# Kernel tuning notes

Hardware: AMD Instinct MI355X
Metric: run time of the kernel (lower is better)

Reference implementation:

```python
import jax, jax.numpy as jnp
import numpy as np

DEPTH = 8          # complete binary tree: 2^8-1 = 255 internal nodes, 256 leaves
N_FEAT = 32
N_CLASSES = 10
BATCH = 131072


def setup_inputs() -> dict:
    key = jax.random.key(0)
    k_x, k_t, k_f, k_c = jax.random.split(key, 4)
    n_internal = (1 << DEPTH) - 1
    n_leaves = 1 << DEPTH
    x = jax.random.normal(k_x, (BATCH, N_FEAT), dtype=jnp.float32)
    # learnable per-node thresholds (initialized from the sklearn tree's thresholds)
    thresholds = jax.random.normal(k_t, (n_internal,), dtype=jnp.float32) * 0.5
    # non-differentiable split feature index per internal node
    feats = jax.random.randint(k_f, (n_internal,), 0, N_FEAT, dtype=jnp.int32)
    # majority class per leaf (argmax of sklearn value array)
    leaf_class = jax.random.randint(k_c, (n_leaves,), 0, N_CLASSES, dtype=jnp.int32)
    return {"x": x, "thresholds": thresholds, "feats": feats, "leaf_class": leaf_class}


def reference(x, thresholds, feats, leaf_class):
    # Soft decision-tree traversal. Internal nodes stored in level (heap) order:
    # level d occupies indices [2^d - 1, 2^(d+1) - 1). Children of the j-th node
    # of a level are the (2j)-th and (2j+1)-th nodes of the next level, so an
    # interleaved stack+reshape reproduces the heap child ordering exactly.
    B = x.shape[0]
    probs = jnp.ones((B, 1), dtype=x.dtype)  # root path probability
    start = 0
    for d in range(DEPTH):
        n = 1 << d
        f = feats[start:start + n]               # [n] split feature per node
        t = thresholds[start:start + n]          # [n] learnable threshold
        act = jax.nn.sigmoid(x[:, f] - t[None, :])   # [B, n] right-branch gate
        # left child gets (1 - act), right child gets act (matches _split_approx)
        probs = jnp.stack([probs * (1.0 - act), probs * act], axis=-1).reshape(B, 2 * n)
        start += n
    # sum leaf path probabilities per majority class (stack + sum in original)
    onehot = jax.nn.one_hot(leaf_class, N_CLASSES, dtype=x.dtype)  # [n_leaves, C]
    p = probs @ onehot                                             # [B, C]
    return p
```

## Files before the change

### kernel.cpp

```cpp
#include <hip/hip_runtime.h>


#define NFEAT 32
#define NCLS  10
#define TPB   256
#define RPB   256
#define XPITCH 258
#define L2E   1.4426950408889634f

typedef _Float16 f16x8 __attribute__((ext_vector_type(8)));
typedef float    f32x4 __attribute__((ext_vector_type(4)));

__device__ __forceinline__ float fexp2(float z) {
#if __has_builtin(__builtin_amdgcn_exp2f)
  return __builtin_amdgcn_exp2f(z);
#else
  return exp2f(z);
#endif
}
__device__ __forceinline__ float frcp(float z) {
#if __has_builtin(__builtin_amdgcn_rcpf)
  return __builtin_amdgcn_rcpf(z);
#else
  return 1.0f / z;
#endif
}
__device__ __forceinline__ float rlf(float v, int lane) {
  return __int_as_float(__builtin_amdgcn_readlane(__float_as_int(v), lane));
}
__device__ __forceinline__ int rli(int v, int lane) {
  return __builtin_amdgcn_readlane(v, lane);
}

struct NodeRegs {
  float ta, tb, t7;
  int   fa, fb, f7;
};

__device__ __forceinline__ void sig2(float tpow, int ft, const float* xT, int rp,
                                     float p0, float p1,
                                     float& l0, float& r0, float& l1, float& r1) {
  const float2 w = *(const float2*)&xT[ft * XPITCH + 2 * rp];
  const float a0 = frcp(__builtin_fmaf(tpow, w.x, 1.0f));
  const float a1 = frcp(__builtin_fmaf(tpow, w.y, 1.0f));
  r0 = p0 * a0;  l0 = p0 - r0;
  r1 = p1 * a1;  l1 = p1 - r1;
}
__device__ __forceinline__ void evalA2(const NodeRegs& R, const float* xT, int n,
                                       int rp, float p0, float p1,
                                       float& l0, float& r0, float& l1, float& r1) {
  sig2(rlf(R.ta, n), rli(R.fa, n), xT, rp, p0, p1, l0, r0, l1, r1);
}
__device__ __forceinline__ void evalB2(const NodeRegs& R, const float* xT, int n,
                                       int rp, float p0, float p1,
                                       float& l0, float& r0, float& l1, float& r1) {
  sig2(rlf(R.tb, n - 63), rli(R.fb, n - 63), xT, rp, p0, p1, l0, r0, l1, r1);
}
__device__ __forceinline__ void leafpair7x2(const NodeRegs& R, const float* xT,
                                            int l7, int rp, float p0, float p1,
                                            unsigned& u0, unsigned& u1) {
  float l0, r0, l1, r1;
  sig2(rlf(R.t7, l7), rli(R.f7, l7), xT, rp, p0, p1, l0, r0, l1, r1);
  const _Float16 hl0 = (_Float16)l0, hr0 = (_Float16)r0;
  const _Float16 hl1 = (_Float16)l1, hr1 = (_Float16)r1;
  u0 = ((unsigned)__builtin_bit_cast(unsigned short, hr0) << 16) |
        (unsigned)__builtin_bit_cast(unsigned short, hl0);
  u1 = ((unsigned)__builtin_bit_cast(unsigned short, hr1) << 16) |
        (unsigned)__builtin_bit_cast(unsigned short, hl1);
}

__device__ __forceinline__ void d5block2(const NodeRegs& R, const float* xT,
                                         int rp, int n5, int l7b,
                                         float p0, float p1,
                                         char* rowp0, char* rowp1,
                                         int boff0, int boff1) {
  float pl0, pr0, pl1, pr1;
  evalA2(R, xT, n5, rp, p0, p1, pl0, pr0, pl1, pr1);
  float qll0, qlr0, qll1, qlr1;
  evalB2(R, xT, 2 * n5 + 1, rp, pl0, pl1, qll0, qlr0, qll1, qlr1);
  float qrl0, qrr0, qrl1, qrr1;
  evalB2(R, xT, 2 * n5 + 2, rp, pr0, pr1, qrl0, qrr0, qrl1, qrr1);
  uint4 u0, u1;
  leafpair7x2(R, xT, l7b + 0, rp, qll0, qll1, u0.x, u1.x);
  leafpair7x2(R, xT, l7b + 1, rp, qlr0, qlr1, u0.y, u1.y);
  leafpair7x2(R, xT, l7b + 2, rp, qrl0, qrl1, u0.z, u1.z);
  leafpair7x2(R, xT, l7b + 3, rp, qrr0, qrr1, u0.w, u1.w);
  *(uint4*)(rowp0 + boff0) = u0;
  *(uint4*)(rowp1 + boff1) = u1;
}

__global__ __launch_bounds__(TPB, 2)
void dt_kernel(const float* __restrict__ x,
               const float* __restrict__ thr,
               const int*   __restrict__ feats,
               const int*   __restrict__ leafc,
               float*       __restrict__ out) {
  __shared__ __align__(16) float s_xT[NFEAT * XPITCH];
  __shared__ __align__(16) char  s_P[RPB * 128];
  __shared__ int s_lc[256];

  const int t    = threadIdx.x;
  const int lane = t & 63;
  const int rp   = t & 127;
  const int h    = t >> 7;

  NodeRegs R;
  R.ta = fexp2(thr[lane] * L2E);
  R.tb = fexp2(thr[63 + lane] * L2E);
  R.t7 = fexp2(thr[127 + 64 * h + lane] * L2E);
  R.fa = feats[lane];
  R.fb = feats[63 + lane];
  R.f7 = feats[127 + 64 * h + lane];

  const float4* xg = (const float4*)x + (size_t)blockIdx.x * (RPB * NFEAT / 4);
#pragma unroll
  for (int k = 0; k < 8; ++k) {
    const int i4 = k * TPB + t;
    const float4 v = xg[i4];
    const int r  = i4 >> 3;
    const int c0 = (i4 & 7) * 4;
    s_xT[(c0 + 0) * XPITCH + r] = fexp2(-v.x * L2E);
    s_xT[(c0 + 1) * XPITCH + r] = fexp2(-v.y * L2E);
    s_xT[(c0 + 2) * XPITCH + r] = fexp2(-v.z * L2E);
    s_xT[(c0 + 3) * XPITCH + r] = fexp2(-v.w * L2E);
  }
  s_lc[t] = leafc[t];

  __syncthreads();

  float pl0, pr0, pl1, pr1;
  evalA2(R, s_xT, 0, rp, 1.0f, 1.0f, pl0, pr0, pl1, pr1);
  const float pd10 = h ? pr0 : pl0;
  const float pd11 = h ? pr1 : pl1;
  evalA2(R, s_xT, 1 + h, rp, pd10, pd11, pl0, pr0, pl1, pr1);
  const float pA0 = pl0, pB0 = pr0, pA1 = pl1, pB1 = pr1;
  float pm00, pm01, pm02, pm03, pm10, pm11, pm12, pm13;
  evalA2(R, s_xT, 3 + 2 * h, rp, pA0, pA1, pm00, pm01, pm10, pm11);
  evalA2(R, s_xT, 4 + 2 * h, rp, pB0, pB1, pm02, pm03, pm12, pm13);

  const int row0 = 2 * rp, row1 = row0 + 1;
  const int swz0 = ((row0 ^ (row0 >> 3)) & 7) << 4;
  const int swz1 = ((row1 ^ (row1 >> 3)) & 7) << 4;
  char* rowp0    = s_P + row0 * 128;
  char* rowp1    = s_P + row1 * 128;
  const int hofs = h * 64;
  const int wv   = t >> 6;
  const int col16 = lane & 15;
  const int kgrpB = (lane >> 4) * 16;

  f32x4 acc[4];
#pragma unroll
  for (int i = 0; i < 4; ++i) acc[i] = (f32x4){0.f, 0.f, 0.f, 0.f};

#pragma unroll 1
  for (int p = 0; p < 4; ++p) {
    __syncthreads();

    const float p30 = (p == 0) ? pm00 : (p == 1) ? pm01 : (p == 2) ? pm02 : pm03;
    const float p31 = (p == 0) ? pm10 : (p == 1) ? pm11 : (p == 2) ? pm12 : pm13;
    const int n3 = 7 + 4 * h + p;
    float p4l0, p4r0, p4l1, p4r1;
    evalA2(R, s_xT, n3, rp, p30, p31, p4l0, p4r0, p4l1, p4r1);
    float q00, q10, q01, q11, q20, q30, q21, q31;
    evalA2(R, s_xT, 2 * n3 + 1, rp, p4l0, p4l1, q00, q10, q01, q11);
    evalA2(R, s_xT, 2 * n3 + 2, rp, p4r0, p4r1, q20, q30, q21, q31);
    const int n5b = 4 * n3 + 3;
#pragma unroll
    for (int s = 0; s < 4; ++s) {
      const float a = (s == 0) ? q00 : (s == 1) ? q10 : (s == 2) ? q20 : q30;
      const float b = (s == 0) ? q01 : (s == 1) ? q11 : (s == 2) ? q21 : q31;
      d5block2(R, s_xT, rp, n5b + s, 16 * p + 4 * s, a, b, rowp0, rowp1,
               (hofs + s * 16) ^ swz0, (hofs + s * 16) ^ swz1);
    }

    __syncthreads();

    f16x8 Bf0, Bf1;
    {
      const int kb = (lane >> 4) * 8;
      const int4 cA0 = *(const int4*)&s_lc[p * 32 + kb];
      const int4 cB0 = *(const int4*)&s_lc[p * 32 + kb + 4];
      uint4 u0;
      u0.x = ((cA0.x == col16) ? 0x3C00u : 0u) | (((cA0.y == col16) ? 0x3C00u : 0u) << 16);
      u0.y = ((cA0.z == col16) ? 0x3C00u : 0u) | (((cA0.w == col16) ? 0x3C00u : 0u) << 16);
      u0.z = ((cB0.x == col16) ? 0x3C00u : 0u) | (((cB0.y == col16) ? 0x3C00u : 0u) << 16);
      u0.w = ((cB0.z == col16) ? 0x3C00u : 0u) | (((cB0.w == col16) ? 0x3C00u : 0u) << 16);
      Bf0 = __builtin_bit_cast(f16x8, u0);
      const int4 cA1 = *(const int4*)&s_lc[128 + p * 32 + kb];
      const int4 cB1 = *(const int4*)&s_lc[128 + p * 32 + kb + 4];
      uint4 u1;
      u1.x = ((cA1.x == col16) ? 0x3C00u : 0u) | (((cA1.y == col16) ? 0x3C00u : 0u) << 16);
      u1.y = ((cA1.z == col16) ? 0x3C00u : 0u) | (((cA1.w == col16) ? 0x3C00u : 0u) << 16);
      u1.z = ((cB1.x == col16) ? 0x3C00u : 0u) | (((cB1.y == col16) ? 0x3C00u : 0u) << 16);
      u1.w = ((cB1.z == col16) ? 0x3C00u : 0u) | (((cB1.w == col16) ? 0x3C00u : 0u) << 16);
      Bf1 = __builtin_bit_cast(f16x8, u1);
    }

#pragma unroll
    for (int i = 0; i < 4; ++i) {
      const int arow = (wv * 4 + i) * 16 + col16;
      const int aswz = ((arow ^ (arow >> 3)) & 7) << 4;
      const char* ap = s_P + arow * 128;
      const f16x8 a0 = *(const f16x8*)(ap + ((kgrpB)      ^ aswz));
      const f16x8 a1 = *(const f16x8*)(ap + ((kgrpB + 64) ^ aswz));
      acc[i] = __builtin_amdgcn_mfma_f32_16x16x32_f16(a0, Bf0, acc[i], 0, 0, 0);
      acc[i] = __builtin_amdgcn_mfma_f32_16x16x32_f16(a1, Bf1, acc[i], 0, 0, 0);
    }
  }

  if (col16 < NCLS) {
    const int r4 = (lane >> 4) * 4;
#pragma unroll
    for (int i = 0; i < 4; ++i) {
      const size_t gr = (size_t)blockIdx.x * RPB + wv * 64 + i * 16 + r4;
#pragma unroll
      for (int j = 0; j < 4; ++j) {
        out[(gr + j) * NCLS + col16] = acc[i][j];
      }
    }
  }
}

extern "C" void kernel_launch(void* const* d_in, const int* in_sizes, int n_in,
                              void* d_out, int out_size, void* d_ws, size_t ws_size,
                              hipStream_t stream) {
  const float* x     = (const float*)d_in[0];
  const float* thr   = (const float*)d_in[1];
  const int*   feats = (const int*)d_in[2];
  const int*   leafc = (const int*)d_in[3];
  float*       out   = (float*)d_out;

  const int B    = in_sizes[0] / NFEAT;
  const int grid = B / RPB;

  dt_kernel<<<grid, TPB, 0, stream>>>(x, thr, feats, leafc, out);
}
```

Measured before the change: 82.54 us.

## Halve rows per block and split tree four ways across waves

Result: no change. 81.07 us (-1.8%).

```diff
diff --git a/kernel.cpp b/kernel.cpp
--- a/kernel.cpp
+++ b/kernel.cpp
@@ -4,8 +4,8 @@
 #define NFEAT 32
 #define NCLS  10
 #define TPB   256
-#define RPB   256
-#define XPITCH 258
+#define RPB   128
+#define XPITCH 130
 #define L2E   1.4426950408889634f
 
 typedef _Float16 f16x8 __attribute__((ext_vector_type(8)));
@@ -69,27 +69,39 @@
         (unsigned)__builtin_bit_cast(unsigned short, hl1);
 }
 
-__device__ __forceinline__ void d5block2(const NodeRegs& R, const float* xT,
-                                         int rp, int n5, int l7b,
+__device__ __forceinline__ void d4block2(const NodeRegs& R, const float* xT,
+                                         int rp, int m, int l7b,
                                          float p0, float p1,
                                          char* rowp0, char* rowp1,
-                                         int boff0, int boff1) {
-  float pl0, pr0, pl1, pr1;
-  evalA2(R, xT, n5, rp, p0, p1, pl0, pr0, pl1, pr1);
-  float qll0, qlr0, qll1, qlr1;
-  evalB2(R, xT, 2 * n5 + 1, rp, pl0, pl1, qll0, qlr0, qll1, qlr1);
-  float qrl0, qrr0, qrl1, qrr1;
-  evalB2(R, xT, 2 * n5 + 2, rp, pr0, pr1, qrl0, qrr0, qrl1, qrr1);
-  uint4 u0, u1;
-  leafpair7x2(R, xT, l7b + 0, rp, qll0, qll1, u0.x, u1.x);
-  leafpair7x2(R, xT, l7b + 1, rp, qlr0, qlr1, u0.y, u1.y);
-  leafpair7x2(R, xT, l7b + 2, rp, qrl0, qrl1, u0.z, u1.z);
-  leafpair7x2(R, xT, l7b + 3, rp, qrr0, qrr1, u0.w, u1.w);
-  *(uint4*)(rowp0 + boff0) = u0;
-  *(uint4*)(rowp1 + boff1) = u1;
-}
-
-__global__ __launch_bounds__(TPB, 2)
+                                         int swz0, int swz1, int qb) {
+  float al0, ar0, al1, ar1;
+  evalA2(R, xT, m, rp, p0, p1, al0, ar0, al1, ar1);
+  float bll0, blr0, bll1, blr1;
+  evalA2(R, xT, 2 * m + 1, rp, al0, al1, bll0, blr0, bll1, blr1);
+  float brl0, brr0, brl1, brr1;
+  evalA2(R, xT, 2 * m + 2, rp, ar0, ar1, brl0, brr0, brl1, brr1);
+  float c0l0, c0r0, c0l1, c0r1, c1l0, c1r0, c1l1, c1r1;
+  float c2l0, c2r0, c2l1, c2r1, c3l0, c3r0, c3l1, c3r1;
+  evalB2(R, xT, 4 * m + 3, rp, bll0, bll1, c0l0, c0r0, c0l1, c0r1);
+  evalB2(R, xT, 4 * m + 4, rp, blr0, blr1, c1l0, c1r0, c1l1, c1r1);
+  evalB2(R, xT, 4 * m + 5, rp, brl0, brl1, c2l0, c2r0, c2l1, c2r1);
+  evalB2(R, xT, 4 * m + 6, rp, brr0, brr1, c3l0, c3r0, c3l1, c3r1);
+  uint4 ua0, ua1, ub0, ub1;
+  leafpair7x2(R, xT, l7b + 0, rp, c0l0, c0l1, ua0.x, ua1.x);
+  leafpair7x2(R, xT, l7b + 1, rp, c0r0, c0r1, ua0.y, ua1.y);
+  leafpair7x2(R, xT, l7b + 2, rp, c1l0, c1l1, ua0.z, ua1.z);
+  leafpair7x2(R, xT, l7b + 3, rp, c1r0, c1r1, ua0.w, ua1.w);
+  leafpair7x2(R, xT, l7b + 4, rp, c2l0, c2l1, ub0.x, ub1.x);
+  leafpair7x2(R, xT, l7b + 5, rp, c2r0, c2r1, ub0.y, ub1.y);
+  leafpair7x2(R, xT, l7b + 6, rp, c3l0, c3l1, ub0.z, ub1.z);
+  leafpair7x2(R, xT, l7b + 7, rp, c3r0, c3r1, ub0.w, ub1.w);
+  *(uint4*)(rowp0 + ((qb)      ^ swz0)) = ua0;
+  *(uint4*)(rowp0 + ((qb + 16) ^ swz0)) = ub0;
+  *(uint4*)(rowp1 + ((qb)      ^ swz1)) = ua1;
+  *(uint4*)(rowp1 + ((qb + 16) ^ swz1)) = ub1;
+}
+
+__global__ __launch_bounds__(TPB, 4)
 void dt_kernel(const float* __restrict__ x,
                const float* __restrict__ thr,
                const int*   __restrict__ feats,
@@ -101,20 +113,20 @@
 
   const int t    = threadIdx.x;
   const int lane = t & 63;
-  const int rp   = t & 127;
-  const int h    = t >> 7;
+  const int rp   = t & 63;
+  const int q    = t >> 6;
 
   NodeRegs R;
   R.ta = fexp2(thr[lane] * L2E);
   R.tb = fexp2(thr[63 + lane] * L2E);
-  R.t7 = fexp2(thr[127 + 64 * h + lane] * L2E);
+  R.t7 = fexp2(thr[127 + 32 * q + (lane & 31)] * L2E);
   R.fa = feats[lane];
   R.fb = feats[63 + lane];
-  R.f7 = feats[127 + 64 * h + lane];
+  R.f7 = feats[127 + 32 * q + (lane & 31)];
 
   const float4* xg = (const float4*)x + (size_t)blockIdx.x * (RPB * NFEAT / 4);
 #pragma unroll
-  for (int k = 0; k < 8; ++k) {
+  for (int k = 0; k < 4; ++k) {
     const int i4 = k * TPB + t;
     const float4 v = xg[i4];
     const int r  = i4 >> 3;
@@ -128,66 +140,56 @@
 
   __syncthreads();
 
-  float pl0, pr0, pl1, pr1;
-  evalA2(R, s_xT, 0, rp, 1.0f, 1.0f, pl0, pr0, pl1, pr1);
-  const float pd10 = h ? pr0 : pl0;
-  const float pd11 = h ? pr1 : pl1;
-  evalA2(R, s_xT, 1 + h, rp, pd10, pd11, pl0, pr0, pl1, pr1);
-  const float pA0 = pl0, pB0 = pr0, pA1 = pl1, pB1 = pr1;
-  float pm00, pm01, pm02, pm03, pm10, pm11, pm12, pm13;
-  evalA2(R, s_xT, 3 + 2 * h, rp, pA0, pA1, pm00, pm01, pm10, pm11);
-  evalA2(R, s_xT, 4 + 2 * h, rp, pB0, pB1, pm02, pm03, pm12, pm13);
+  float l0, r0, l1, r1;
+  evalA2(R, s_xT, 0, rp, 1.0f, 1.0f, l0, r0, l1, r1);
+  const float P1_0 = (q < 2) ? l0 : r0;
+  const float P1_1 = (q < 2) ? l1 : r1;
+  evalA2(R, s_xT, 1 + (q >> 1), rp, P1_0, P1_1, l0, r0, l1, r1);
+  const float P2_0 = (q & 1) ? r0 : l0;
+  const float P2_1 = (q & 1) ? r1 : l1;
+  evalA2(R, s_xT, 3 + q, rp, P2_0, P2_1, l0, r0, l1, r1);
+  const float P3L0 = l0, P3R0 = r0, P3L1 = l1, P3R1 = r1;
+  float p40_0, p41_0, p42_0, p43_0, p40_1, p41_1, p42_1, p43_1;
+  evalA2(R, s_xT, 7 + 2 * q, rp, P3L0, P3L1, p40_0, p41_0, p40_1, p41_1);
+  evalA2(R, s_xT, 8 + 2 * q, rp, P3R0, P3R1, p42_0, p43_0, p42_1, p43_1);
 
   const int row0 = 2 * rp, row1 = row0 + 1;
   const int swz0 = ((row0 ^ (row0 >> 3)) & 7) << 4;
   const int swz1 = ((row1 ^ (row1 >> 3)) & 7) << 4;
   char* rowp0    = s_P + row0 * 128;
   char* rowp1    = s_P + row1 * 128;
-  const int hofs = h * 64;
-  const int wv   = t >> 6;
+  const int qb   = 32 * q;
   const int col16 = lane & 15;
   const int kgrpB = (lane >> 4) * 16;
 
-  f32x4 acc[4];
-#pragma unroll
-  for (int i = 0; i < 4; ++i) acc[i] = (f32x4){0.f, 0.f, 0.f, 0.f};
+  f32x4 acc0 = {0.f, 0.f, 0.f, 0.f};
+  f32x4 acc1 = {0.f, 0.f, 0.f, 0.f};
 
 #pragma unroll 1
   for (int p = 0; p < 4; ++p) {
     __syncthreads();
 
-    const float p30 = (p == 0) ? pm00 : (p == 1) ? pm01 : (p == 2) ? pm02 : pm03;
-    const float p31 = (p == 0) ? pm10 : (p == 1) ? pm11 : (p == 2) ? pm12 : pm13;
-    const int n3 = 7 + 4 * h + p;
-    float p4l0, p4r0, p4l1, p4r1;
-    evalA2(R, s_xT, n3, rp, p30, p31, p4l0, p4r0, p4l1, p4r1);
-    float q00, q10, q01, q11, q20, q30, q21, q31;
-    evalA2(R, s_xT, 2 * n3 + 1, rp, p4l0, p4l1, q00, q10, q01, q11);
-    evalA2(R, s_xT, 2 * n3 + 2, rp, p4r0, p4r1, q20, q30, q21, q31);
-    const int n5b = 4 * n3 + 3;
-#pragma unroll
-    for (int s = 0; s < 4; ++s) {
-      const float a = (s == 0) ? q00 : (s == 1) ? q10 : (s == 2) ? q20 : q30;
-      const float b = (s == 0) ? q01 : (s == 1) ? q11 : (s == 2) ? q21 : q31;
-      d5block2(R, s_xT, rp, n5b + s, 16 * p + 4 * s, a, b, rowp0, rowp1,
-               (hofs + s * 16) ^ swz0, (hofs + s * 16) ^ swz1);
-    }
+    const float A0 = (p == 0) ? p40_0 : (p == 1) ? p41_0 : (p == 2) ? p42_0 : p43_0;
+    const float A1 = (p == 0) ? p40_1 : (p == 1) ? p41_1 : (p == 2) ? p42_1 : p43_1;
+    d4block2(R, s_xT, rp, 15 + 4 * q + p, 8 * p, A0, A1,
+             rowp0, rowp1, swz0, swz1, qb);
 
     __syncthreads();
 
     f16x8 Bf0, Bf1;
     {
-      const int kb = (lane >> 4) * 8;
-      const int4 cA0 = *(const int4*)&s_lc[p * 32 + kb];
-      const int4 cB0 = *(const int4*)&s_lc[p * 32 + kb + 4];
+      const int kb   = (lane >> 4) * 8;
+      const int base = 64 * (kb >> 4) + 16 * p + (kb & 8);
+      const int4 cA0 = *(const int4*)&s_lc[base];
+      const int4 cB0 = *(const int4*)&s_lc[base + 4];
       uint4 u0;
       u0.x = ((cA0.x == col16) ? 0x3C00u : 0u) | (((cA0.y == col16) ? 0x3C00u : 0u) << 16);
       u0.y = ((cA0.z == col16) ? 0x3C00u : 0u) | (((cA0.w == col16) ? 0x3C00u : 0u) << 16);
       u0.z = ((cB0.x == col16) ? 0x3C00u : 0u) | (((cB0.y == col16) ? 0x3C00u : 0u) << 16);
       u0.w = ((cB0.z == col16) ? 0x3C00u : 0u) | (((cB0.w == col16) ? 0x3C00u : 0u) << 16);
       Bf0 = __builtin_bit_cast(f16x8, u0);
-      const int4 cA1 = *(const int4*)&s_lc[128 + p * 32 + kb];
-      const int4 cB1 = *(const int4*)&s_lc[128 + p * 32 + kb + 4];
+      const int4 cA1 = *(const int4*)&s_lc[128 + base];
+      const int4 cB1 = *(const int4*)&s_lc[128 + base + 4];
       uint4 u1;
       u1.x = ((cA1.x == col16) ? 0x3C00u : 0u) | (((cA1.y == col16) ? 0x3C00u : 0u) << 16);
       u1.y = ((cA1.z == col16) ? 0x3C00u : 0u) | (((cA1.w == col16) ? 0x3C00u : 0u) << 16);
@@ -197,25 +199,30 @@
     }
 
 #pragma unroll
-    for (int i = 0; i < 4; ++i) {
-      const int arow = (wv * 4 + i) * 16 + col16;
+    for (int i = 0; i < 2; ++i) {
+      const int arow = (q * 2 + i) * 16 + col16;
       const int aswz = ((arow ^ (arow >> 3)) & 7) << 4;
       const char* ap = s_P + arow * 128;
       const f16x8 a0 = *(const f16x8*)(ap + ((kgrpB)      ^ aswz));
       const f16x8 a1 = *(const f16x8*)(ap + ((kgrpB + 64) ^ aswz));
-      acc[i] = __builtin_amdgcn_mfma_f32_16x16x32_f16(a0, Bf0, acc[i], 0, 0, 0);
-      acc[i] = __builtin_amdgcn_mfma_f32_16x16x32_f16(a1, Bf1, acc[i], 0, 0, 0);
+      if (i == 0) {
+        acc0 = __builtin_amdgcn_mfma_f32_16x16x32_f16(a0, Bf0, acc0, 0, 0, 0);
+        acc0 = __builtin_amdgcn_mfma_f32_16x16x32_f16(a1, Bf1, acc0, 0, 0, 0);
+      } else {
+        acc1 = __builtin_amdgcn_mfma_f32_16x16x32_f16(a0, Bf0, acc1, 0, 0, 0);
+        acc1 = __builtin_amdgcn_mfma_f32_16x16x32_f16(a1, Bf1, acc1, 0, 0, 0);
+      }
     }
   }
 
   if (col16 < NCLS) {
     const int r4 = (lane >> 4) * 4;
 #pragma unroll
-    for (int i = 0; i < 4; ++i) {
-      const size_t gr = (size_t)blockIdx.x * RPB + wv * 64 + i * 16 + r4;
+    for (int i = 0; i < 2; ++i) {
+      const size_t gr = (size_t)blockIdx.x * RPB + (q * 2 + i) * 16 + r4;
 #pragma unroll
       for (int j = 0; j < 4; ++j) {
-        out[(gr + j) * NCLS + col16] = acc[i][j];
+        out[(gr + j) * NCLS + col16] = (i == 0) ? acc0[j] : acc1[j];
       }
     }
   }
```
